# Kernel tuning notes

Hardware: AMD Instinct MI355X
Metric: run time of the kernel (lower is better)

The kernel has to match this reference:

```python
import jax, jax.numpy as jnp
import numpy as np

SR = 16000
GATE_SMOOTH_WIN = max(1, int(1.0 * 0.001 * SR))  # 16 samples


def _gate(x, W1, b1, W2, b2):
    """Input-dependent gate gamma_t in [0,1]. x: (B, L) -> (B, L, 1)."""
    h = jax.nn.silu(x[..., None] * W1[:, 0] + b1)          # (B, L, GH)
    gamma = jax.nn.sigmoid(h @ W2.T + b2)                   # (B, L, 1)
    win = GATE_SMOOTH_WIN
    if win > 1:  # moving-average smoothing with reflect padding (matches F.pad+conv1d)
        pad = win // 2
        L = x.shape[1]
        g = jnp.pad(gamma, ((0, 0), (pad, pad), (0, 0)), mode='reflect')
        cs = jnp.cumsum(g, axis=1)
        cs = jnp.pad(cs, ((0, 0), (1, 0), (0, 0)))
        sm = (cs[:, win:, :] - cs[:, :-win, :]) / win       # (B, L+1, 1)
        gamma = sm[:, :L, :]
    return gamma


def setup_inputs() -> dict:
    key = jax.random.key(0)
    ks = jax.random.split(key, 5)
    B, L, D, GH = 8, 32768, 64, 16
    x = jax.random.normal(ks[0], (B, L), dtype=jnp.float32)

    # Mel-spaced frequency init (matches _mel_spaced)
    def hz_to_mel(f):
        return 2595.0 * np.log10(1.0 + f / 700.0)

    def mel_to_hz(m):
        return 700.0 * (10.0 ** (m / 2595.0) - 1.0)

    mels = np.linspace(hz_to_mel(80.0), hz_to_mel(8000.0), D)
    freqs_hz = mel_to_hz(mels)
    omega = jnp.asarray(2.0 * np.pi * freqs_hz / SR, dtype=jnp.float32)

    window_samples = 25.0 * 0.001 * SR
    alpha_init = -5.0 / window_samples
    raw_alpha = jnp.full((D,), np.float32(np.log(np.expm1(-alpha_init))), dtype=jnp.float32)
    b_real = jnp.full((D,), np.float32(1.0 / np.sqrt(D)), dtype=jnp.float32)
    b_imag = jnp.zeros((D,), dtype=jnp.float32)

    W1 = jax.random.normal(ks[1], (GH, 1), dtype=jnp.float32)
    b1 = jax.random.normal(ks[2], (GH,), dtype=jnp.float32) * 0.1
    W2 = jax.random.normal(ks[3], (1, GH), dtype=jnp.float32) * 0.1  # randomized so gate varies
    b2 = jnp.full((1,), 2.0, dtype=jnp.float32)
    return dict(x=x, omega=omega, raw_alpha=raw_alpha, b_real=b_real, b_imag=b_imag,
                W1=W1, b1=b1, W2=W2, b2=b2)


def reference(x, omega, raw_alpha, b_real, b_imag, W1, b1, W2, b2):
    B, L = x.shape
    alpha = -jax.nn.softplus(raw_alpha)
    a = jnp.exp(jax.lax.complex(alpha, omega))        # (D,) complex64, |a| < 1
    b = jax.lax.complex(b_real, b_imag)               # (D,) complex64
    gamma = _gate(x, W1, b1, W2, b2)                  # (B, L, 1)

    xc = x.astype(jnp.complex64)
    gT = jnp.moveaxis(gamma, 1, 0)                    # (L, B, 1)
    xT = jnp.moveaxis(xc, 1, 0)                       # (L, B)

    def step(h, inp):
        g_t, x_t = inp                                # (B,1) float, (B,) complex
        h = g_t * a * h + b * x_t[:, None]            # (B, D) complex64
        return h, h

    h0 = jnp.zeros((B, omega.shape[0]), dtype=jnp.complex64)
    _, H = jax.lax.scan(step, h0, (gT, xT))           # (L, B, D)
    return jnp.moveaxis(H, 0, 1)                      # (B, L, D) complex64
```

## Files before the change

kernel.cpp:

```cpp
#include <hip/hip_runtime.h>
#include <math.h>

#define BB 8
#define LL 32768
#define DD 64
#define GH 16
#define TC 128
#define NC (LL / TC)
#define BD (BB * DD)
#define WIN 16
#define PAD 8

typedef float f32x2 __attribute__((ext_vector_type(2)));

__device__ __forceinline__ float sig_(float z) { return 1.0f / (1.0f + expf(-z)); }

__device__ __forceinline__ float raw_gate(float xv, const float* w1, const float* bb1,
                                          const float* w2, float bb2) {
    float h = bb2;
#pragma unroll
    for (int i = 0; i < GH; i++) {
        const float z = xv * w1[i] + bb1[i];
        h += (z * sig_(z)) * w2[i];
    }
    return sig_(h);
}

__global__ __launch_bounds__(256) void gate_kernel(
        const float* __restrict__ x,
        const float* __restrict__ W1, const float* __restrict__ b1,
        const float* __restrict__ W2, const float* __restrict__ b2,
        float* __restrict__ gw) {
    __shared__ float sraw[256 + WIN];
    const int tilesPerB = LL / 256;
    const int b  = blockIdx.x / tilesPerB;
    const int t0 = (blockIdx.x % tilesPerB) * 256;

    float w1[GH], bb1[GH], w2[GH];
#pragma unroll
    for (int i = 0; i < GH; i++) { w1[i] = W1[i]; bb1[i] = b1[i]; w2[i] = W2[i]; }
    const float bb2 = b2[0];

    for (int j = threadIdx.x; j < 256 + WIN; j += 256) {
        int idx = t0 - PAD + j;
        if (idx < 0)    idx = -idx;
        if (idx >= LL)  idx = 2 * LL - 2 - idx;
        sraw[j] = raw_gate(x[b * LL + idx], w1, bb1, w2, bb2);
    }
    __syncthreads();

    float acc = 0.0f;
#pragma unroll
    for (int k = 0; k < WIN; k++) acc += sraw[threadIdx.x + k];
    gw[b * LL + t0 + threadIdx.x] = acc * (1.0f / WIN);
}

__device__ __forceinline__ void chan_params(const float* omega, const float* raw_alpha,
                                            int d, float& ar, float& ai) {
    const float alpha = -log1pf(expf(raw_alpha[d]));
    const float r = expf(alpha);
    ar = r * cosf(omega[d]);
    ai = r * sinf(omega[d]);
}

__global__ __launch_bounds__(256) void chunk_reduce_kernel(
        const float* __restrict__ x, const float* __restrict__ gw,
        const float* __restrict__ omega, const float* __restrict__ raw_alpha,
        const float* __restrict__ b_real, const float* __restrict__ b_imag,
        float4* __restrict__ ps) {
    const int tid = blockIdx.x * blockDim.x + threadIdx.x;
    const int d = tid & (DD - 1);
    const int u = tid >> 6;
    const int b = u / NC;
    const int c = u % NC;

    float ar, ai;
    chan_params(omega, raw_alpha, d, ar, ai);
    const float br = b_real[d], bi = b_imag[d];

    float Pr = 1.0f, Pi = 0.0f, Sr = 0.0f, Si = 0.0f;
    const float4* xb4 = (const float4*)(x  + b * LL + c * TC);
    const float4* gb4 = (const float4*)(gw + b * LL + c * TC);
#pragma unroll 2
    for (int q = 0; q < TC / 4; q++) {
        const float4 g4 = gb4[q];
        const float4 x4 = xb4[q];
        const float gs[4] = {g4.x, g4.y, g4.z, g4.w};
        const float xs[4] = {x4.x, x4.y, x4.z, x4.w};
#pragma unroll
        for (int j = 0; j < 4; j++) {
            const float cr = gs[j] * ar, ci = gs[j] * ai;
            const float nPr = cr * Pr - ci * Pi;
            const float nPi = cr * Pi + ci * Pr;
            const float nSr = cr * Sr - ci * Si + br * xs[j];
            const float nSi = cr * Si + ci * Sr + bi * xs[j];
            Pr = nPr; Pi = nPi; Sr = nSr; Si = nSi;
        }
    }
    ps[(b * DD + d) * NC + c] = make_float4(Pr, Pi, Sr, Si);
}

__global__ __launch_bounds__(256) void carry_scan_kernel(
        const float4* __restrict__ ps, float2* __restrict__ hin) {
    const int w    = blockIdx.x * (blockDim.x >> 6) + (threadIdx.x >> 6);
    const int lane = threadIdx.x & 63;
    const int c0   = lane * 4;

    float4 v[4];
#pragma unroll
    for (int j = 0; j < 4; j++) v[j] = ps[w * NC + c0 + j];

    float Pr = 1.0f, Pi = 0.0f, Sr = 0.0f, Si = 0.0f;
#pragma unroll
    for (int j = 0; j < 4; j++) {
        const float pr = v[j].x, pi = v[j].y, sr = v[j].z, si = v[j].w;
        const float nPr = pr * Pr - pi * Pi;
        const float nPi = pr * Pi + pi * Pr;
        const float nSr = pr * Sr - pi * Si + sr;
        const float nSi = pr * Si + pi * Sr + si;
        Pr = nPr; Pi = nPi; Sr = nSr; Si = nSi;
    }

#pragma unroll
    for (int off = 1; off < 64; off <<= 1) {
        const float pPr = __shfl_up(Pr, off, 64);
        const float pPi = __shfl_up(Pi, off, 64);
        const float pSr = __shfl_up(Sr, off, 64);
        const float pSi = __shfl_up(Si, off, 64);
        if (lane >= off) {
            const float nPr = Pr * pPr - Pi * pPi;
            const float nPi = Pr * pPi + Pi * pPr;
            const float nSr = Pr * pSr - Pi * pSi + Sr;
            const float nSi = Pr * pSi + Pi * pSr + Si;
            Pr = nPr; Pi = nPi; Sr = nSr; Si = nSi;
        }
    }

    float hr = __shfl_up(Sr, 1, 64);
    float hi = __shfl_up(Si, 1, 64);
    if (lane == 0) { hr = 0.0f; hi = 0.0f; }

#pragma unroll
    for (int j = 0; j < 4; j++) {
        hin[(c0 + j) * BD + w] = make_float2(hr, hi);
        const float pr = v[j].x, pi = v[j].y, sr = v[j].z, si = v[j].w;
        const float nhr = pr * hr - pi * hi + sr;
        const float nhi = pr * hi + pi * hr + si;
        hr = nhr; hi = nhi;
    }
}

template <bool CPLX>
__global__ __launch_bounds__(256) void expand_kernel(
        const float* __restrict__ x, const float* __restrict__ gw,
        const float* __restrict__ omega, const float* __restrict__ raw_alpha,
        const float* __restrict__ b_real, const float* __restrict__ b_imag,
        const float2* __restrict__ hin, float* __restrict__ out) {
    const int tid = blockIdx.x * blockDim.x + threadIdx.x;
    const int d = tid & (DD - 1);
    const int u = tid >> 6;
    const int b = u / NC;
    const int c = u % NC;

    float ar, ai;
    chan_params(omega, raw_alpha, d, ar, ai);
    const float br = b_real[d], bi = b_imag[d];

    const float2 h0 = hin[c * BD + (b * DD + d)];
    float hr = h0.x, hi = h0.y;

    const float4* xb4 = (const float4*)(x  + b * LL + c * TC);
    const float4* gb4 = (const float4*)(gw + b * LL + c * TC);
    const size_t base = (size_t)(b * LL + c * TC) * DD + d;

#pragma unroll 2
    for (int q = 0; q < TC / 4; q++) {
        const float4 g4 = gb4[q];
        const float4 x4 = xb4[q];
        const float gs[4] = {g4.x, g4.y, g4.z, g4.w};
        const float xs[4] = {x4.x, x4.y, x4.z, x4.w};
#pragma unroll
        for (int j = 0; j < 4; j++) {
            const float cr = gs[j] * ar, ci = gs[j] * ai;
            const float nhr = cr * hr - ci * hi + br * xs[j];
            const float nhi = cr * hi + ci * hr + bi * xs[j];
            hr = nhr; hi = nhi;
            const size_t e = base + (size_t)(q * 4 + j) * DD;
            if constexpr (CPLX) {
                f32x2 val; val.x = hr; val.y = hi;
                __builtin_nontemporal_store(val, (f32x2*)out + e);
            } else {
                __builtin_nontemporal_store(hr, out + e);
            }
        }
    }
}

template <bool CPLX>
__global__ __launch_bounds__(64) void fallback_kernel(
        const float* __restrict__ x,
        const float* __restrict__ omega, const float* __restrict__ raw_alpha,
        const float* __restrict__ b_real, const float* __restrict__ b_imag,
        const float* __restrict__ W1, const float* __restrict__ b1,
        const float* __restrict__ W2, const float* __restrict__ b2,
        float* __restrict__ out) {
    const int b = blockIdx.x;
    const int d = threadIdx.x;

    __shared__ float xtile[64];
    __shared__ float sraw[64 + WIN];
    __shared__ float gsm[64];

    float w1[GH], bb1[GH], w2[GH];
#pragma unroll
    for (int i = 0; i < GH; i++) { w1[i] = W1[i]; bb1[i] = b1[i]; w2[i] = W2[i]; }
    const float bb2 = b2[0];

    float ar, ai;
    chan_params(omega, raw_alpha, d, ar, ai);
    const float br = b_real[d], bi = b_imag[d];

    float hr = 0.0f, hi = 0.0f;
    for (int t0 = 0; t0 < LL; t0 += 64) {
        __syncthreads();
        for (int j = threadIdx.x; j < 64 + WIN; j += 64) {
            int idx = t0 - PAD + j;
            if (idx < 0)   idx = -idx;
            if (idx >= LL) idx = 2 * LL - 2 - idx;
            sraw[j] = raw_gate(x[b * LL + idx], w1, bb1, w2, bb2);
        }
        xtile[threadIdx.x] = x[b * LL + t0 + threadIdx.x];
        __syncthreads();
        float acc = 0.0f;
#pragma unroll
        for (int k = 0; k < WIN; k++) acc += sraw[threadIdx.x + k];
        gsm[threadIdx.x] = acc * (1.0f / WIN);
        __syncthreads();
        for (int tt = 0; tt < 64; tt++) {
            const float g  = gsm[tt];
            const float xv = xtile[tt];
            const float cr = g * ar, ci = g * ai;
            const float nhr = cr * hr - ci * hi + br * xv;
            const float nhi = cr * hi + ci * hr + bi * xv;
            hr = nhr; hi = nhi;
            const size_t e = (size_t)(b * LL + t0 + tt) * DD + d;
            if constexpr (CPLX) {
                f32x2 val; val.x = hr; val.y = hi;
                ((f32x2*)out)[e] = val;
            } else {
                out[e] = hr;
            }
        }
    }
}

extern "C" void kernel_launch(void* const* d_in, const int* in_sizes, int n_in,
                              void* d_out, int out_size, void* d_ws, size_t ws_size,
                              hipStream_t stream) {
    const float* x         = (const float*)d_in[0];
    const float* omega     = (const float*)d_in[1];
    const float* raw_alpha = (const float*)d_in[2];
    const float* b_real    = (const float*)d_in[3];
    const float* b_imag    = (const float*)d_in[4];
    const float* W1        = (const float*)d_in[5];
    const float* b1        = (const float*)d_in[6];
    const float* W2        = (const float*)d_in[7];
    const float* b2        = (const float*)d_in[8];

    float* out = (float*)d_out;

    const long long NOUT = (long long)BB * LL * DD;
    const bool cplx = ((long long)out_size == 2 * NOUT);

    const size_t WSNEED = (size_t)BB * LL * 4 + (size_t)BD * NC * 16 + (size_t)BD * NC * 8;

    if (ws_size >= WSNEED) {
        float*  ws  = (float*)d_ws;
        float*  gw  = ws;
        float4* ps  = (float4*)(ws + BB * LL);
        float2* hin = (float2*)(ws + BB * LL + BD * NC * 4);

        gate_kernel<<<BB * (LL / 256), 256, 0, stream>>>(x, W1, b1, W2, b2, gw);
        chunk_reduce_kernel<<<(BD * NC) / 256, 256, 0, stream>>>(x, gw, omega, raw_alpha,
                                                                 b_real, b_imag, ps);
        carry_scan_kernel<<<BD / 4, 256, 0, stream>>>(ps, hin);
        if (cplx) {
            expand_kernel<true><<<(BD * NC) / 256, 256, 0, stream>>>(
                x, gw, omega, raw_alpha, b_real, b_imag, hin, out);
        } else {
            expand_kernel<false><<<(BD * NC) / 256, 256, 0, stream>>>(
                x, gw, omega, raw_alpha, b_real, b_imag, hin, out);
        }
    } else {
        if (cplx) {
            fallback_kernel<true><<<BB, 64, 0, stream>>>(
                x, omega, raw_alpha, b_real, b_imag, W1, b1, W2, b2, out);
        } else {
            fallback_kernel<false><<<BB, 64, 0, stream>>>(
                x, omega, raw_alpha, b_real, b_imag, W1, b1, W2, b2, out);
        }
    }
}
```

Measured before the change: 116.5 us.

## Fuse gate, chunk reduce, carry scan and expand into one cooperative kernel

Replaces the four-kernel pipeline with a single cooperative kernel of 512 blocks. Each block computes the smoothed gate and caches x in shared memory, reduces its chunks, then uses grid-wide syncs to run the carry scan and expand. This removes three launch boundaries and the round trip of the gate array through global memory. In exchange it adds two grid barriers and depends on all 512 blocks being co-resident, falling back to the old path if the cooperative launch fails.

```diff
diff --git a/kernel.cpp b/kernel.cpp
--- a/kernel.cpp
+++ b/kernel.cpp
@@ -1,5 +1,8 @@
 #include <hip/hip_runtime.h>
+#include <hip/hip_cooperative_groups.h>
 #include <math.h>
+
+namespace cg = cooperative_groups;
 
 #define BB 8
 #define LL 32768
@@ -10,6 +13,8 @@
 #define BD (BB * DD)
 #define WIN 16
 #define PAD 8
+#define TBLK 512
+#define NBLK 512
 
 typedef float f32x2 __attribute__((ext_vector_type(2)));
 
@@ -24,6 +29,153 @@
         h += (z * sig_(z)) * w2[i];
     }
     return sig_(h);
+}
+
+__device__ __forceinline__ void chan_params(const float* omega, const float* raw_alpha,
+                                            int d, float& ar, float& ai) {
+    const float alpha = -log1pf(expf(raw_alpha[d]));
+    const float r = expf(alpha);
+    ar = r * cosf(omega[d]);
+    ai = r * sinf(omega[d]);
+}
+
+template <bool CPLX>
+__global__ __launch_bounds__(256, 2) void fused_kernel(
+        const float* __restrict__ x,
+        const float* __restrict__ omega, const float* __restrict__ raw_alpha,
+        const float* __restrict__ b_real, const float* __restrict__ b_imag,
+        const float* __restrict__ W1, const float* __restrict__ b1,
+        const float* __restrict__ W2, const float* __restrict__ b2,
+        float4* __restrict__ ps, float2* __restrict__ hin,
+        float* __restrict__ out) {
+    __shared__ float xt[TBLK + WIN];
+    __shared__ float sraw[TBLK + WIN];
+    __shared__ float gsm[TBLK];
+
+    const int k    = blockIdx.x;
+    const int b    = k >> 6;
+    const int c4   = k & 63;
+    const int t0   = c4 * TBLK;
+    const int tid  = threadIdx.x;
+    const int lane = tid & 63;
+    const int wv   = tid >> 6;
+
+    {
+        float w1[GH], bb1[GH], w2[GH];
+#pragma unroll
+        for (int i = 0; i < GH; i++) { w1[i] = W1[i]; bb1[i] = b1[i]; w2[i] = W2[i]; }
+        const float bb2 = b2[0];
+        for (int j = tid; j < TBLK + WIN; j += 256) {
+            int idx = t0 - PAD + j;
+            if (idx < 0)   idx = -idx;
+            if (idx >= LL) idx = 2 * LL - 2 - idx;
+            const float xv = x[b * LL + idx];
+            xt[j] = xv;
+            sraw[j] = raw_gate(xv, w1, bb1, w2, bb2);
+        }
+    }
+    __syncthreads();
+    for (int i = tid; i < TBLK; i += 256) {
+        float acc = 0.0f;
+#pragma unroll
+        for (int kk = 0; kk < WIN; kk++) acc += sraw[i + kk];
+        gsm[i] = acc * (1.0f / WIN);
+    }
+    __syncthreads();
+
+    float ar, ai;
+    chan_params(omega, raw_alpha, lane, ar, ai);
+    const float br = b_real[lane], bi = b_imag[lane];
+
+    {
+        float Pr = 1.0f, Pi = 0.0f, Sr = 0.0f, Si = 0.0f;
+        const int lo = wv * TC;
+#pragma unroll 4
+        for (int t = 0; t < TC; t++) {
+            const float g  = gsm[lo + t];
+            const float xv = xt[lo + t + PAD];
+            const float cr = g * ar, ci = g * ai;
+            const float nPr = cr * Pr - ci * Pi;
+            const float nPi = cr * Pi + ci * Pr;
+            const float nSr = cr * Sr - ci * Si + br * xv;
+            const float nSi = cr * Si + ci * Sr + bi * xv;
+            Pr = nPr; Pi = nPi; Sr = nSr; Si = nSi;
+        }
+        const int c = c4 * 4 + wv;
+        ps[(b * DD + lane) * NC + c] = make_float4(Pr, Pi, Sr, Si);
+    }
+    __threadfence();
+    cg::this_grid().sync();
+
+    if (k < 128) {
+        const int w  = k * 4 + wv;
+        const int c0 = lane * 4;
+        float4 v[4];
+#pragma unroll
+        for (int j = 0; j < 4; j++) v[j] = ps[w * NC + c0 + j];
+
+        float Pr = 1.0f, Pi = 0.0f, Sr = 0.0f, Si = 0.0f;
+#pragma unroll
+        for (int j = 0; j < 4; j++) {
+            const float pr = v[j].x, pi = v[j].y, sr = v[j].z, si = v[j].w;
+            const float nPr = pr * Pr - pi * Pi;
+            const float nPi = pr * Pi + pi * Pr;
+            const float nSr = pr * Sr - pi * Si + sr;
+            const float nSi = pr * Si + pi * Sr + si;
+            Pr = nPr; Pi = nPi; Sr = nSr; Si = nSi;
+        }
+#pragma unroll
+        for (int off = 1; off < 64; off <<= 1) {
+            const float pPr = __shfl_up(Pr, off, 64);
+            const float pPi = __shfl_up(Pi, off, 64);
+            const float pSr = __shfl_up(Sr, off, 64);
+            const float pSi = __shfl_up(Si, off, 64);
+            if (lane >= off) {
+                const float nPr = Pr * pPr - Pi * pPi;
+                const float nPi = Pr * pPi + Pi * pPr;
+                const float nSr = Pr * pSr - Pi * pSi + Sr;
+                const float nSi = Pr * pSi + Pi * pSr + Si;
+                Pr = nPr; Pi = nPi; Sr = nSr; Si = nSi;
+            }
+        }
+        float hr = __shfl_up(Sr, 1, 64);
+        float hi = __shfl_up(Si, 1, 64);
+        if (lane == 0) { hr = 0.0f; hi = 0.0f; }
+#pragma unroll
+        for (int j = 0; j < 4; j++) {
+            hin[(c0 + j) * BD + w] = make_float2(hr, hi);
+            const float pr = v[j].x, pi = v[j].y, sr = v[j].z, si = v[j].w;
+            const float nhr = pr * hr - pi * hi + sr;
+            const float nhi = pr * hi + pi * hr + si;
+            hr = nhr; hi = nhi;
+        }
+    }
+    __threadfence();
+    cg::this_grid().sync();
+
+    {
+        const int c = c4 * 4 + wv;
+        const float2 h0 = hin[c * BD + b * DD + lane];
+        float hr = h0.x, hi = h0.y;
+        const int lo = wv * TC;
+        size_t e = (size_t)(b * LL + t0 + lo) * DD + lane;
+#pragma unroll 4
+        for (int t = 0; t < TC; t++) {
+            const float g  = gsm[lo + t];
+            const float xv = xt[lo + t + PAD];
+            const float cr = g * ar, ci = g * ai;
+            const float nhr = cr * hr - ci * hi + br * xv;
+            const float nhi = cr * hi + ci * hr + bi * xv;
+            hr = nhr; hi = nhi;
+            if constexpr (CPLX) {
+                f32x2 val; val.x = hr; val.y = hi;
+                __builtin_nontemporal_store(val, (f32x2*)out + e);
+            } else {
+                __builtin_nontemporal_store(hr, out + e);
+            }
+            e += DD;
+        }
+    }
 }
 
 __global__ __launch_bounds__(256) void gate_kernel(
@@ -53,14 +205,6 @@
 #pragma unroll
     for (int k = 0; k < WIN; k++) acc += sraw[threadIdx.x + k];
     gw[b * LL + t0 + threadIdx.x] = acc * (1.0f / WIN);
-}
-
-__device__ __forceinline__ void chan_params(const float* omega, const float* raw_alpha,
-                                            int d, float& ar, float& ai) {
-    const float alpha = -log1pf(expf(raw_alpha[d]));
-    const float r = expf(alpha);
-    ar = r * cosf(omega[d]);
-    ai = r * sinf(omega[d]);
 }
 
 __global__ __launch_bounds__(256) void chunk_reduce_kernel(
@@ -120,7 +264,6 @@
         const float nSi = pr * Si + pi * Sr + si;
         Pr = nPr; Pi = nPi; Sr = nSr; Si = nSi;
     }
-
 #pragma unroll
     for (int off = 1; off < 64; off <<= 1) {
         const float pPr = __shfl_up(Pr, off, 64);
@@ -135,11 +278,9 @@
             Pr = nPr; Pi = nPi; Sr = nSr; Si = nSi;
         }
     }
-
     float hr = __shfl_up(Sr, 1, 64);
     float hi = __shfl_up(Si, 1, 64);
     if (lane == 0) { hr = 0.0f; hi = 0.0f; }
-
 #pragma unroll
     for (int j = 0; j < 4; j++) {
         hin[(c0 + j) * BD + w] = make_float2(hr, hi);
@@ -272,8 +413,23 @@
     const long long NOUT = (long long)BB * LL * DD;
     const bool cplx = ((long long)out_size == 2 * NOUT);
 
+    const size_t PS_BYTES  = (size_t)BD * NC * sizeof(float4);
+    const size_t HIN_BYTES = (size_t)BD * NC * sizeof(float2);
+    if (ws_size >= PS_BYTES + HIN_BYTES) {
+        float4* ps  = (float4*)d_ws;
+        float2* hin = (float2*)((char*)d_ws + PS_BYTES);
+        void* args[] = {(void*)&x, (void*)&omega, (void*)&raw_alpha, (void*)&b_real,
+                        (void*)&b_imag, (void*)&W1, (void*)&b1, (void*)&W2, (void*)&b2,
+                        (void*)&ps, (void*)&hin, (void*)&out};
+        const void* fn = cplx ? (const void*)&fused_kernel<true>
+                              : (const void*)&fused_kernel<false>;
+        hipError_t err = hipLaunchCooperativeKernel(fn, dim3(NBLK), dim3(256),
+                                                    args, 0, stream);
+        if (err == hipSuccess) return;
+        (void)hipGetLastError();
+    }
+
     const size_t WSNEED = (size_t)BB * LL * 4 + (size_t)BD * NC * 16 + (size_t)BD * NC * 8;
-
     if (ws_size >= WSNEED) {
         float*  ws  = (float*)d_ws;
         float*  gw  = ws;
```

New measurement: 322.0 us. +176.3%, slower.

## Fuse gate into scan kernels and merge carry scan via last-block atomic

Applied to the files above, without the earlier changes.

Removes the standalone gate kernel and recomputes the smoothed gate per chunk in shared memory inside both the reduce and expand kernels. The carry scan kernel is folded into the reduce kernel: an atomic counter per batch lets the last-finishing block run the cross-chunk scan. This cuts launches and the global round trip of the gate array. In exchange the gate is computed twice and the carry scan is serialized onto one block per batch.

```diff
diff --git a/kernel.cpp b/kernel.cpp
--- a/kernel.cpp
+++ b/kernel.cpp
@@ -10,6 +10,8 @@
 #define BD (BB * DD)
 #define WIN 16
 #define PAD 8
+#define WPB 4
+#define NBLK (BB * NC / WPB)
 
 typedef float f32x2 __attribute__((ext_vector_type(2)));
 
@@ -24,35 +26,6 @@
         h += (z * sig_(z)) * w2[i];
     }
     return sig_(h);
-}
-
-__global__ __launch_bounds__(256) void gate_kernel(
-        const float* __restrict__ x,
-        const float* __restrict__ W1, const float* __restrict__ b1,
-        const float* __restrict__ W2, const float* __restrict__ b2,
-        float* __restrict__ gw) {
-    __shared__ float sraw[256 + WIN];
-    const int tilesPerB = LL / 256;
-    const int b  = blockIdx.x / tilesPerB;
-    const int t0 = (blockIdx.x % tilesPerB) * 256;
-
-    float w1[GH], bb1[GH], w2[GH];
-#pragma unroll
-    for (int i = 0; i < GH; i++) { w1[i] = W1[i]; bb1[i] = b1[i]; w2[i] = W2[i]; }
-    const float bb2 = b2[0];
-
-    for (int j = threadIdx.x; j < 256 + WIN; j += 256) {
-        int idx = t0 - PAD + j;
-        if (idx < 0)    idx = -idx;
-        if (idx >= LL)  idx = 2 * LL - 2 - idx;
-        sraw[j] = raw_gate(x[b * LL + idx], w1, bb1, w2, bb2);
-    }
-    __syncthreads();
-
-    float acc = 0.0f;
-#pragma unroll
-    for (int k = 0; k < WIN; k++) acc += sraw[threadIdx.x + k];
-    gw[b * LL + t0 + threadIdx.x] = acc * (1.0f / WIN);
 }
 
 __device__ __forceinline__ void chan_params(const float* omega, const float* raw_alpha,
@@ -63,136 +36,169 @@
     ai = r * sinf(omega[d]);
 }
 
-__global__ __launch_bounds__(256) void chunk_reduce_kernel(
-        const float* __restrict__ x, const float* __restrict__ gw,
+__device__ __forceinline__ void stage_gate_x(
+        const float* __restrict__ x, int b, int t0, int lane,
+        const float* __restrict__ W1, const float* __restrict__ b1,
+        const float* __restrict__ W2, const float* __restrict__ b2,
+        float* __restrict__ sraw, float* __restrict__ gsm, float* __restrict__ xt) {
+    float w1[GH], bb1[GH], w2[GH];
+#pragma unroll
+    for (int i = 0; i < GH; i++) { w1[i] = W1[i]; bb1[i] = b1[i]; w2[i] = W2[i]; }
+    const float bb2 = b2[0];
+    for (int j = lane; j < TC + WIN; j += 64) {
+        int idx = t0 - PAD + j;
+        if (idx < 0)   idx = -idx;
+        if (idx >= LL) idx = 2 * LL - 2 - idx;
+        const float xv = x[b * LL + idx];
+        sraw[j] = raw_gate(xv, w1, bb1, w2, bb2);
+        if (j >= PAD && j < PAD + TC) xt[j - PAD] = xv;
+    }
+    for (int i = lane; i < TC; i += 64) {
+        float acc = 0.0f;
+#pragma unroll
+        for (int k = 0; k < WIN; k++) acc += sraw[i + k];
+        gsm[i] = acc * (1.0f / WIN);
+    }
+}
+
+__global__ __launch_bounds__(256) void reduce_carry_kernel(
+        const float* __restrict__ x,
         const float* __restrict__ omega, const float* __restrict__ raw_alpha,
         const float* __restrict__ b_real, const float* __restrict__ b_imag,
-        float4* __restrict__ ps) {
-    const int tid = blockIdx.x * blockDim.x + threadIdx.x;
-    const int d = tid & (DD - 1);
-    const int u = tid >> 6;
-    const int b = u / NC;
-    const int c = u % NC;
+        const float* __restrict__ W1, const float* __restrict__ b1,
+        const float* __restrict__ W2, const float* __restrict__ b2,
+        float4* __restrict__ ps, float2* __restrict__ hin,
+        unsigned int* __restrict__ ctr) {
+    __shared__ float sraw[WPB][TC + WIN];
+    __shared__ float gsm[WPB][TC];
+    __shared__ float xt[WPB][TC];
+    __shared__ int lastflag;
+
+    const int tid  = threadIdx.x;
+    const int lane = tid & 63;
+    const int wv   = tid >> 6;
+    const int u    = blockIdx.x * WPB + wv;
+    const int b    = u / NC;
+    const int c    = u & (NC - 1);
+    const int t0   = c * TC;
+
+    stage_gate_x(x, b, t0, lane, W1, b1, W2, b2, sraw[wv], gsm[wv], xt[wv]);
 
     float ar, ai;
-    chan_params(omega, raw_alpha, d, ar, ai);
-    const float br = b_real[d], bi = b_imag[d];
+    chan_params(omega, raw_alpha, lane, ar, ai);
+    const float br = b_real[lane], bi = b_imag[lane];
 
     float Pr = 1.0f, Pi = 0.0f, Sr = 0.0f, Si = 0.0f;
-    const float4* xb4 = (const float4*)(x  + b * LL + c * TC);
-    const float4* gb4 = (const float4*)(gw + b * LL + c * TC);
-#pragma unroll 2
-    for (int q = 0; q < TC / 4; q++) {
-        const float4 g4 = gb4[q];
-        const float4 x4 = xb4[q];
-        const float gs[4] = {g4.x, g4.y, g4.z, g4.w};
-        const float xs[4] = {x4.x, x4.y, x4.z, x4.w};
-#pragma unroll
-        for (int j = 0; j < 4; j++) {
-            const float cr = gs[j] * ar, ci = gs[j] * ai;
-            const float nPr = cr * Pr - ci * Pi;
-            const float nPi = cr * Pi + ci * Pr;
-            const float nSr = cr * Sr - ci * Si + br * xs[j];
-            const float nSi = cr * Si + ci * Sr + bi * xs[j];
-            Pr = nPr; Pi = nPi; Sr = nSr; Si = nSi;
-        }
-    }
-    ps[(b * DD + d) * NC + c] = make_float4(Pr, Pi, Sr, Si);
-}
-
-__global__ __launch_bounds__(256) void carry_scan_kernel(
-        const float4* __restrict__ ps, float2* __restrict__ hin) {
-    const int w    = blockIdx.x * (blockDim.x >> 6) + (threadIdx.x >> 6);
-    const int lane = threadIdx.x & 63;
-    const int c0   = lane * 4;
-
-    float4 v[4];
-#pragma unroll
-    for (int j = 0; j < 4; j++) v[j] = ps[w * NC + c0 + j];
-
-    float Pr = 1.0f, Pi = 0.0f, Sr = 0.0f, Si = 0.0f;
-#pragma unroll
-    for (int j = 0; j < 4; j++) {
-        const float pr = v[j].x, pi = v[j].y, sr = v[j].z, si = v[j].w;
-        const float nPr = pr * Pr - pi * Pi;
-        const float nPi = pr * Pi + pi * Pr;
-        const float nSr = pr * Sr - pi * Si + sr;
-        const float nSi = pr * Si + pi * Sr + si;
+#pragma unroll 4
+    for (int t = 0; t < TC; t++) {
+        const float g  = gsm[wv][t];
+        const float xv = xt[wv][t];
+        const float cr = g * ar, ci = g * ai;
+        const float nPr = cr * Pr - ci * Pi;
+        const float nPi = cr * Pi + ci * Pr;
+        const float nSr = cr * Sr - ci * Si + br * xv;
+        const float nSi = cr * Si + ci * Sr + bi * xv;
         Pr = nPr; Pi = nPi; Sr = nSr; Si = nSi;
     }
-
-#pragma unroll
-    for (int off = 1; off < 64; off <<= 1) {
-        const float pPr = __shfl_up(Pr, off, 64);
-        const float pPi = __shfl_up(Pi, off, 64);
-        const float pSr = __shfl_up(Sr, off, 64);
-        const float pSi = __shfl_up(Si, off, 64);
-        if (lane >= off) {
-            const float nPr = Pr * pPr - Pi * pPi;
-            const float nPi = Pr * pPi + Pi * pPr;
-            const float nSr = Pr * pSr - Pi * pSi + Sr;
-            const float nSi = Pr * pSi + Pi * pSr + Si;
-            Pr = nPr; Pi = nPi; Sr = nSr; Si = nSi;
-        }
-    }
-
-    float hr = __shfl_up(Sr, 1, 64);
-    float hi = __shfl_up(Si, 1, 64);
-    if (lane == 0) { hr = 0.0f; hi = 0.0f; }
-
-#pragma unroll
-    for (int j = 0; j < 4; j++) {
-        hin[(c0 + j) * BD + w] = make_float2(hr, hi);
-        const float pr = v[j].x, pi = v[j].y, sr = v[j].z, si = v[j].w;
-        const float nhr = pr * hr - pi * hi + sr;
-        const float nhi = pr * hi + pi * hr + si;
-        hr = nhr; hi = nhi;
+    ps[c * BD + b * DD + lane] = make_float4(Pr, Pi, Sr, Si);
+
+    __threadfence();
+    __syncthreads();
+    if (tid == 0) lastflag = (atomicAdd(&ctr[b], 1u) == 63u) ? 1 : 0;
+    __syncthreads();
+    if (lastflag) {
+        __threadfence();
+        for (int dd = wv * 16; dd < wv * 16 + 16; dd++) {
+            const int chain = b * DD + dd;
+            const int c0 = lane * 4;
+            float4 v[4];
+#pragma unroll
+            for (int j = 0; j < 4; j++) v[j] = ps[(c0 + j) * BD + chain];
+
+            float Qr = 1.0f, Qi = 0.0f, Tr = 0.0f, Ti = 0.0f;
+#pragma unroll
+            for (int j = 0; j < 4; j++) {
+                const float pr = v[j].x, pi = v[j].y, sr = v[j].z, si = v[j].w;
+                const float nQr = pr * Qr - pi * Qi;
+                const float nQi = pr * Qi + pi * Qr;
+                const float nTr = pr * Tr - pi * Ti + sr;
+                const float nTi = pr * Ti + pi * Tr + si;
+                Qr = nQr; Qi = nQi; Tr = nTr; Ti = nTi;
+            }
+#pragma unroll
+            for (int off = 1; off < 64; off <<= 1) {
+                const float pQr = __shfl_up(Qr, off, 64);
+                const float pQi = __shfl_up(Qi, off, 64);
+                const float pTr = __shfl_up(Tr, off, 64);
+                const float pTi = __shfl_up(Ti, off, 64);
+                if (lane >= off) {
+                    const float nQr = Qr * pQr - Qi * pQi;
+                    const float nQi = Qr * pQi + Qi * pQr;
+                    const float nTr = Qr * pTr - Qi * pTi + Tr;
+                    const float nTi = Qr * pTi + Qi * pTr + Ti;
+                    Qr = nQr; Qi = nQi; Tr = nTr; Ti = nTi;
+                }
+            }
+            float hr = __shfl_up(Tr, 1, 64);
+            float hi = __shfl_up(Ti, 1, 64);
+            if (lane == 0) { hr = 0.0f; hi = 0.0f; }
+#pragma unroll
+            for (int j = 0; j < 4; j++) {
+                hin[(c0 + j) * BD + chain] = make_float2(hr, hi);
+                const float pr = v[j].x, pi = v[j].y, sr = v[j].z, si = v[j].w;
+                const float nhr = pr * hr - pi * hi + sr;
+                const float nhi = pr * hi + pi * hr + si;
+                hr = nhr; hi = nhi;
+            }
+        }
     }
 }
 
 template <bool CPLX>
-__global__ __launch_bounds__(256) void expand_kernel(
-        const float* __restrict__ x, const float* __restrict__ gw,
+__global__ __launch_bounds__(256) void expand2_kernel(
+        const float* __restrict__ x,
         const float* __restrict__ omega, const float* __restrict__ raw_alpha,
         const float* __restrict__ b_real, const float* __restrict__ b_imag,
+        const float* __restrict__ W1, const float* __restrict__ b1,
+        const float* __restrict__ W2, const float* __restrict__ b2,
         const float2* __restrict__ hin, float* __restrict__ out) {
-    const int tid = blockIdx.x * blockDim.x + threadIdx.x;
-    const int d = tid & (DD - 1);
-    const int u = tid >> 6;
-    const int b = u / NC;
-    const int c = u % NC;
+    __shared__ float sraw[WPB][TC + WIN];
+    __shared__ float gsm[WPB][TC];
+    __shared__ float xt[WPB][TC];
+
+    const int tid  = threadIdx.x;
+    const int lane = tid & 63;
+    const int wv   = tid >> 6;
+    const int u    = blockIdx.x * WPB + wv;
+    const int b    = u / NC;
+    const int c    = u & (NC - 1);
+    const int t0   = c * TC;
+
+    stage_gate_x(x, b, t0, lane, W1, b1, W2, b2, sraw[wv], gsm[wv], xt[wv]);
 
     float ar, ai;
-    chan_params(omega, raw_alpha, d, ar, ai);
-    const float br = b_real[d], bi = b_imag[d];
-
-    const float2 h0 = hin[c * BD + (b * DD + d)];
+    chan_params(omega, raw_alpha, lane, ar, ai);
+    const float br = b_real[lane], bi = b_imag[lane];
+
+    const float2 h0 = hin[c * BD + b * DD + lane];
     float hr = h0.x, hi = h0.y;
 
-    const float4* xb4 = (const float4*)(x  + b * LL + c * TC);
-    const float4* gb4 = (const float4*)(gw + b * LL + c * TC);
-    const size_t base = (size_t)(b * LL + c * TC) * DD + d;
-
-#pragma unroll 2
-    for (int q = 0; q < TC / 4; q++) {
-        const float4 g4 = gb4[q];
-        const float4 x4 = xb4[q];
-        const float gs[4] = {g4.x, g4.y, g4.z, g4.w};
-        const float xs[4] = {x4.x, x4.y, x4.z, x4.w};
-#pragma unroll
-        for (int j = 0; j < 4; j++) {
-            const float cr = gs[j] * ar, ci = gs[j] * ai;
-            const float nhr = cr * hr - ci * hi + br * xs[j];
-            const float nhi = cr * hi + ci * hr + bi * xs[j];
-            hr = nhr; hi = nhi;
-            const size_t e = base + (size_t)(q * 4 + j) * DD;
-            if constexpr (CPLX) {
-                f32x2 val; val.x = hr; val.y = hi;
-                __builtin_nontemporal_store(val, (f32x2*)out + e);
-            } else {
-                __builtin_nontemporal_store(hr, out + e);
-            }
-        }
+    size_t e = (size_t)(b * LL + t0) * DD + lane;
+#pragma unroll 4
+    for (int t = 0; t < TC; t++) {
+        const float g  = gsm[wv][t];
+        const float xv = xt[wv][t];
+        const float cr = g * ar, ci = g * ai;
+        const float nhr = cr * hr - ci * hi + br * xv;
+        const float nhi = cr * hi + ci * hr + bi * xv;
+        hr = nhr; hi = nhi;
+        if constexpr (CPLX) {
+            f32x2 val; val.x = hr; val.y = hi;
+            __builtin_nontemporal_store(val, (f32x2*)out + e);
+        } else {
+            __builtin_nontemporal_store(hr, out + e);
+        }
+        e += DD;
     }
 }
 
@@ -272,24 +278,24 @@
     const long long NOUT = (long long)BB * LL * DD;
     const bool cplx = ((long long)out_size == 2 * NOUT);
 
-    const size_t WSNEED = (size_t)BB * LL * 4 + (size_t)BD * NC * 16 + (size_t)BD * NC * 8;
-
-    if (ws_size >= WSNEED) {
-        float*  ws  = (float*)d_ws;
-        float*  gw  = ws;
-        float4* ps  = (float4*)(ws + BB * LL);
-        float2* hin = (float2*)(ws + BB * LL + BD * NC * 4);
-
-        gate_kernel<<<BB * (LL / 256), 256, 0, stream>>>(x, W1, b1, W2, b2, gw);
-        chunk_reduce_kernel<<<(BD * NC) / 256, 256, 0, stream>>>(x, gw, omega, raw_alpha,
-                                                                 b_real, b_imag, ps);
-        carry_scan_kernel<<<BD / 4, 256, 0, stream>>>(ps, hin);
+    const size_t PS_BYTES  = (size_t)NC * BD * sizeof(float4);
+    const size_t HIN_BYTES = (size_t)NC * BD * sizeof(float2);
+    const size_t CTR_BYTES = BB * sizeof(unsigned int);
+
+    if (ws_size >= PS_BYTES + HIN_BYTES + CTR_BYTES) {
+        float4* ps        = (float4*)d_ws;
+        float2* hin       = (float2*)((char*)d_ws + PS_BYTES);
+        unsigned int* ctr = (unsigned int*)((char*)d_ws + PS_BYTES + HIN_BYTES);
+
+        hipMemsetAsync(ctr, 0, CTR_BYTES, stream);
+        reduce_carry_kernel<<<NBLK, 256, 0, stream>>>(
+            x, omega, raw_alpha, b_real, b_imag, W1, b1, W2, b2, ps, hin, ctr);
         if (cplx) {
-            expand_kernel<true><<<(BD * NC) / 256, 256, 0, stream>>>(
-                x, gw, omega, raw_alpha, b_real, b_imag, hin, out);
+            expand2_kernel<true><<<NBLK, 256, 0, stream>>>(
+                x, omega, raw_alpha, b_real, b_imag, W1, b1, W2, b2, hin, out);
         } else {
-            expand_kernel<false><<<(BD * NC) / 256, 256, 0, stream>>>(
-                x, gw, omega, raw_alpha, b_real, b_imag, hin, out);
+            expand2_kernel<false><<<NBLK, 256, 0, stream>>>(
+                x, omega, raw_alpha, b_real, b_imag, W1, b1, W2, b2, hin, out);
         }
     } else {
         if (cplx) {
```

Measured after the change: 198.5 us. 1.7x slower.
